# Kernel tuning notes

Measured on AMD Instinct MI355X. Metric: run time of the kernel, lower is better.

The kernel has to match this reference:

```python
import jax, jax.numpy as jnp
import numpy as np
import math

NUM_HEADS = 16

def get_slopes(n):
    def pow2(n):
        start = 2 ** (-2 ** (-(math.log2(n) - 3)))
        return [start * start ** i for i in range(n)]
    if math.log2(n).is_integer():
        return pow2(n)
    c = 2 ** math.floor(math.log2(n))
    return pow2(c) + get_slopes(2 * c)[0::2][: n - c]


def setup_inputs() -> dict:
    key = jax.random.key(0)
    ks = jax.random.split(key, 5)
    B, T, C = 2, 2048, 1024
    return {
        "x": jax.random.normal(ks[0], (B, T, C), dtype=jnp.float32),
        "W_qkv": jax.random.normal(ks[1], (C, 3 * C), dtype=jnp.float32) * 0.02,
        "b_qkv": jax.random.normal(ks[2], (3 * C,), dtype=jnp.float32) * 0.02,
        "W_proj": jax.random.normal(ks[3], (C, C), dtype=jnp.float32) * 0.02,
        "b_proj": jax.random.normal(ks[4], (C,), dtype=jnp.float32) * 0.02,
    }


def reference(x, W_qkv, b_qkv, W_proj, b_proj):
    B, T, C = x.shape
    H = NUM_HEADS
    D = C // H
    qkv = x @ W_qkv + b_qkv                       # [B,T,3C]
    q, k, v = jnp.split(qkv, 3, axis=-1)
    q = q.reshape(B, T, H, D).transpose(0, 2, 1, 3)  # [B,H,T,D]
    k = k.reshape(B, T, H, D).transpose(0, 2, 1, 3)
    v = v.reshape(B, T, H, D).transpose(0, 2, 1, 3)

    slopes = jnp.asarray(get_slopes(H), dtype=jnp.float32)  # [H]
    idx = jnp.arange(T)
    # alibi_bias(L).T in source: -(i-j) for j<=i, 0 for j>i  == min(j-i, 0)
    alibi = jnp.minimum(idx[None, :] - idx[:, None], 0).astype(jnp.float32)  # [T,T]
    bias = slopes[:, None, None] * alibi          # [H,T,T]

    scale = 1.0 / math.sqrt(D)
    scores = jnp.einsum("bhtd,bhsd->bhts", q, k) * scale + bias[None]
    # NOTE: source code builds a causal -inf mask but never adds it -> non-causal
    w = jax.nn.softmax(scores, axis=-1)
    y = jnp.einsum("bhts,bhsd->bhtd", w, v)       # [B,H,T,D]
    y = y.transpose(0, 2, 1, 3).reshape(B, T, C)
    return y @ W_proj + b_proj
```

## Files before the change

### kernel.cpp

```cpp
#include <hip/hip_runtime.h>
#include <hip/hip_bf16.h>
#include <cmath>
#include <cstdint>

typedef __bf16 bf16_t;
typedef __bf16 bf16x8 __attribute__((ext_vector_type(8)));
typedef float f32x4 __attribute__((ext_vector_type(4)));
typedef float f32x8 __attribute__((ext_vector_type(8)));

static_assert(sizeof(bf16x8) == 16, "bf16x8 must be 16B");

#define MFMA16(a, b, c) __builtin_amdgcn_mfma_f32_16x16x32_bf16((a), (b), (c), 0, 0, 0)

__device__ __forceinline__ void load_lds_16B(const bf16_t* gsrc, bf16_t* ldst) {
  __builtin_amdgcn_global_load_lds(
      (const __attribute__((address_space(1))) void*)gsrc,
      (__attribute__((address_space(3))) void*)ldst, 16, 0, 0);
}

__global__ void detect_dtype(const unsigned short* __restrict__ x,
                             int* __restrict__ flag) {
  const int lane = threadIdx.x;
  int cnt = 0;
#pragma unroll
  for (int t = 0; t < 8; ++t) {
    unsigned short u = x[2 * (lane + 64 * t)];
    int e = (u >> 7) & 0xFF;
    cnt += (e >= 90 && e <= 130) ? 1 : 0;
  }
#pragma unroll
  for (int off = 1; off < 64; off <<= 1) cnt += __shfl_xor(cnt, off, 64);
  if (lane == 0) *flag = (cnt < 300) ? 1 : 0;
}

__global__ __launch_bounds__(256) void convert_x(const void* __restrict__ x_,
                                                 bf16_t* __restrict__ xb,
                                                 const int* __restrict__ flagp) {
  const size_t idx = ((size_t)blockIdx.x * 256 + threadIdx.x) * 8;
  if (*flagp) {
    f32x8 v = *(const f32x8*)((const float*)x_ + idx);
    bf16x8 bv;
#pragma unroll
    for (int e = 0; e < 8; ++e) bv[e] = (bf16_t)v[e];
    *(bf16x8*)&xb[idx] = bv;
  } else {
    *(bf16x8*)&xb[idx] = *(const bf16x8*)((const bf16_t*)x_ + idx);
  }
}

__global__ __launch_bounds__(256) void wt_transpose(const void* __restrict__ W_,
                                                    bf16_t* __restrict__ Wt,
                                                    int K, int N,
                                                    const int* __restrict__ flagp) {
  __shared__ bf16_t tile[64 * 72];
  const int is_f32 = *flagp;
  const int tid = threadIdx.x;
  const int k0 = blockIdx.y * 64;
  const int n0 = blockIdx.x * 64;
  const int r = tid >> 3;
  const int c = (tid & 7) * 8;
#pragma unroll
  for (int t = 0; t < 2; ++t) {
    int rr = r + t * 32;
    if (is_f32) {
      const float* W = (const float*)W_;
      f32x8 v = *(const f32x8*)&W[(size_t)(k0 + rr) * N + n0 + c];
      bf16x8 bv;
#pragma unroll
      for (int e = 0; e < 8; ++e) bv[e] = (bf16_t)v[e];
      *(bf16x8*)&tile[rr * 72 + c] = bv;
    } else {
      const bf16_t* W = (const bf16_t*)W_;
      *(bf16x8*)&tile[rr * 72 + c] = *(const bf16x8*)&W[(size_t)(k0 + rr) * N + n0 + c];
    }
  }
  __syncthreads();
#pragma unroll
  for (int t = 0; t < 2; ++t) {
    int rr = r + t * 32;
    bf16x8 v;
#pragma unroll
    for (int e = 0; e < 8; ++e) v[e] = tile[(c + e) * 72 + rr];
    *(bf16x8*)&Wt[(size_t)(n0 + rr) * K + k0 + c] = v;
  }
}

__global__ __launch_bounds__(256, 2) void gemm_bt(
    const bf16_t* __restrict__ A, const bf16_t* __restrict__ Bt,
    const void* __restrict__ bias_, void* __restrict__ C_,
    bf16_t* __restrict__ qb, bf16_t* __restrict__ kb, bf16_t* __restrict__ vt,
    int M, int N, int K, int mode, const int* __restrict__ flagp) {
  __shared__ bf16_t As[128 * 64];
  __shared__ bf16_t Bs[128 * 64];
  const int is_f32 = *flagp;
  const int tid = threadIdx.x;
  const int wave = tid >> 6, lane = tid & 63;
  const int l16 = lane & 15, quad = lane >> 4;
  const int m0 = blockIdx.y * 128, n0 = blockIdx.x * 128;
  const int wm = (wave >> 1) * 64, wn = (wave & 1) * 64;
  const int lr = lane >> 3, lc = (lane & 7) * 8;
  f32x4 acc[4][4] = {};

  for (int k0 = 0; k0 < K; k0 += 64) {
#pragma unroll
    for (int t = 0; t < 4; ++t) {
      const int chunk = wave * 4 + t;
      const int row = chunk * 8 + lr;
      load_lds_16B(&A[(size_t)(m0 + row) * K + k0 + lc], &As[chunk * 512]);
      load_lds_16B(&Bt[(size_t)(n0 + row) * K + k0 + lc], &Bs[chunk * 512]);
    }
    __syncthreads();
#pragma unroll
    for (int ks = 0; ks < 2; ++ks) {
      bf16x8 af[4], bfr[4];
#pragma unroll
      for (int i = 0; i < 4; ++i) {
        af[i]  = *(const bf16x8*)&As[(wm + i * 16 + l16) * 64 + ks * 32 + quad * 8];
        bfr[i] = *(const bf16x8*)&Bs[(wn + i * 16 + l16) * 64 + ks * 32 + quad * 8];
      }
#pragma unroll
      for (int i = 0; i < 4; ++i)
#pragma unroll
        for (int j = 0; j < 4; ++j)
          acc[i][j] = MFMA16(af[i], bfr[j], acc[i][j]);
    }
    __syncthreads();
  }

#pragma unroll
  for (int j = 0; j < 4; ++j) {
    const int n = n0 + wn + j * 16 + l16;
    const float bv = is_f32 ? ((const float*)bias_)[n]
                            : (float)((const bf16_t*)bias_)[n];
    if (mode == 0) {
#pragma unroll
      for (int i = 0; i < 4; ++i)
#pragma unroll
        for (int r = 0; r < 4; ++r) {
          int m = m0 + wm + i * 16 + quad * 4 + r;
          float val = acc[i][j][r] + bv;
          if (is_f32) ((float*)C_)[(size_t)m * N + n] = val;
          else ((bf16_t*)C_)[(size_t)m * N + n] = (bf16_t)val;
        }
    } else {
      const int region = n >> 10;
      const int nn = n & 1023;
      const int hh = nn >> 6, dd = nn & 63;
#pragma unroll
      for (int i = 0; i < 4; ++i)
#pragma unroll
        for (int r = 0; r < 4; ++r) {
          int m = m0 + wm + i * 16 + quad * 4 + r;
          int bb = m >> 11, tt = m & 2047;
          size_t bh = (size_t)(bb * 16 + hh);
          float val = acc[i][j][r] + bv;
          if (region == 0)
            qb[(bh * 2048 + tt) * 64 + dd] = (bf16_t)val;
          else if (region == 1)
            kb[(bh * 2048 + tt) * 64 + dd] = (bf16_t)val;
          else
            vt[bh * 131072 + (size_t)dd * 2048 + tt] = (bf16_t)val;
        }
    }
  }
}

__global__ __launch_bounds__(512, 4) void attn_kernel(
    const bf16_t* __restrict__ qbuf, const bf16_t* __restrict__ kbuf,
    const bf16_t* __restrict__ vT, bf16_t* __restrict__ y) {
  const int T = 2048;
  __shared__ __align__(16) char smem[57344];
  bf16_t* Ks  = (bf16_t*)smem;
  bf16_t* VTs = (bf16_t*)(smem + 18432);
  bf16_t* Ps  = (bf16_t*)(smem + 36864);

  const int tid = threadIdx.x;
  const int wave = tid >> 6, lane = tid & 63;
  const int g2 = wave >> 2, wp = wave & 3;
  const int l16 = lane & 15, quad = lane >> 4;
  const int bh = blockIdx.y;
  const int b = bh >> 4, h = bh & 15;
  const int i0 = blockIdx.x * 128 + wp * 32;
  const float L2E = 1.44269504088896f;
  const float c1 = 0.125f * L2E;
  const float c2 = exp2f(-0.5f * (float)(h + 1)) * L2E;

  bf16x8 qf[2][2];
#pragma unroll
  for (int g = 0; g < 2; ++g) {
    const bf16_t* qrow = qbuf + ((size_t)bh * T + i0 + g * 16 + l16) * 64;
    qf[g][0] = *(const bf16x8*)&qrow[quad * 8];
    qf[g][1] = *(const bf16x8*)&qrow[32 + quad * 8];
  }

  f32x4 o[2][4] = {};
  float rsum[2][4] = {};

  const bf16_t* kbase = kbuf + (size_t)bh * T * 64;
  const bf16_t* vbase = vT + (size_t)bh * 64 * T;

  bf16_t* myKs = Ks + g2 * 4608;
  bf16_t* myVs = VTs + g2 * 4608;
  bf16_t* Pw = Ps + wave * 1280;

  const int gtid = tid & 255;
  const int sr = gtid >> 3, sc = (gtid & 7) * 8;
  const int jbase = g2 * 1024;

  for (int jj = 0; jj < 1024; jj += 64) {
    const int j0 = jbase + jj;
#pragma unroll
    for (int t = 0; t < 2; ++t) {
      int rr = sr + t * 32;
      *(bf16x8*)&myKs[rr * 72 + sc] = *(const bf16x8*)&kbase[(size_t)(j0 + rr) * 64 + sc];
      *(bf16x8*)&myVs[rr * 72 + sc] = *(const bf16x8*)&vbase[(size_t)rr * T + j0 + sc];
    }
    __syncthreads();

#pragma unroll
    for (int hl = 0; hl < 2; ++hl) {
      bf16x8 kf[2][2];
#pragma unroll
      for (int jtl = 0; jtl < 2; ++jtl) {
        const int jr = (hl * 2 + jtl) * 16 + l16;
        kf[jtl][0] = *(const bf16x8*)&myKs[jr * 72 + quad * 8];
        kf[jtl][1] = *(const bf16x8*)&myKs[jr * 72 + 32 + quad * 8];
      }
#pragma unroll
      for (int g = 0; g < 2; ++g) {
        f32x4 s[2] = {};
#pragma unroll
        for (int jtl = 0; jtl < 2; ++jtl) {
          s[jtl] = MFMA16(qf[g][0], kf[jtl][0], s[jtl]);
          s[jtl] = MFMA16(qf[g][1], kf[jtl][1], s[jtl]);
        }
        const float fb = (float)(i0 + g * 16 + quad * 4);
#pragma unroll
        for (int jtl = 0; jtl < 2; ++jtl) {
          const float jmf = (float)(j0 + (hl * 2 + jtl) * 16 + l16);
#pragma unroll
          for (int r = 0; r < 4; ++r) {
            float dm = fminf(jmf - (fb + (float)r), 0.0f);
            float p = exp2f(c1 * s[jtl][r] + c2 * dm);
            rsum[g][r] += p;
            Pw[(g * 16 + quad * 4 + r) * 40 + jtl * 16 + l16] = (bf16_t)p;
          }
        }
      }
      __asm__ volatile("s_waitcnt lgkmcnt(0)" ::: "memory");

      bf16x8 vf[4];
#pragma unroll
      for (int dt = 0; dt < 4; ++dt)
        vf[dt] = *(const bf16x8*)&myVs[(dt * 16 + l16) * 72 + hl * 32 + quad * 8];
#pragma unroll
      for (int g = 0; g < 2; ++g) {
        const bf16x8 pf = *(const bf16x8*)&Pw[(g * 16 + l16) * 40 + quad * 8];
#pragma unroll
        for (int dt = 0; dt < 4; ++dt)
          o[g][dt] = MFMA16(pf, vf[dt], o[g][dt]);
      }
    }
    __syncthreads();
  }

#pragma unroll
  for (int g = 0; g < 2; ++g)
#pragma unroll
    for (int r = 0; r < 4; ++r) {
      float s = rsum[g][r];
      s += __shfl_xor(s, 1, 64);
      s += __shfl_xor(s, 2, 64);
      s += __shfl_xor(s, 4, 64);
      s += __shfl_xor(s, 8, 64);
      rsum[g][r] = s;
    }

  __syncthreads();
  float* exO = (float*)smem;
  float* exR = (float*)(smem + 36864);
  if (g2 == 1) {
    float* myO = exO + wp * (32 * 65);
#pragma unroll
    for (int g = 0; g < 2; ++g)
#pragma unroll
      for (int dt = 0; dt < 4; ++dt)
#pragma unroll
        for (int r = 0; r < 4; ++r)
          myO[(g * 16 + quad * 4 + r) * 65 + dt * 16 + l16] = o[g][dt][r];
    if (l16 == 0) {
#pragma unroll
      for (int g = 0; g < 2; ++g)
#pragma unroll
        for (int r = 0; r < 4; ++r)
          exR[wp * 32 + g * 16 + quad * 4 + r] = rsum[g][r];
    }
  }
  __syncthreads();
  if (g2 == 0) {
    float* myO = exO + wp * (32 * 65);
#pragma unroll
    for (int g = 0; g < 2; ++g)
#pragma unroll
      for (int dt = 0; dt < 4; ++dt)
#pragma unroll
        for (int r = 0; r < 4; ++r) {
          const int row = g * 16 + quad * 4 + r;
          const float denom = rsum[g][r] + exR[wp * 32 + row];
          const float val = (o[g][dt][r] + myO[row * 65 + dt * 16 + l16]) / denom;
          const int ig = i0 + row;
          const int d = dt * 16 + l16;
          y[((size_t)(b * 2048 + ig)) * 1024 + h * 64 + d] = (bf16_t)val;
        }
  }
}

extern "C" void kernel_launch(void* const* d_in, const int* in_sizes, int n_in,
                              void* d_out, int out_size, void* d_ws, size_t ws_size,
                              hipStream_t stream) {
  const void* x     = d_in[0];
  const void* Wqkv  = d_in[1];
  const void* bqkv  = d_in[2];
  const void* Wproj = d_in[3];
  const void* bproj = d_in[4];

  const size_t SEG = (size_t)32 * 2048 * 64;
  bf16_t* ws = (bf16_t*)d_ws;
  bf16_t* qb = ws;
  bf16_t* kb = ws + SEG;
  bf16_t* vt = ws + 2 * SEG;
  bf16_t* yb = ws + 3 * SEG;
  bf16_t* WqkvT  = yb;
  bf16_t* WprojT = qb;
  bf16_t* xb = (bf16_t*)d_out;
  int* flag1 = (int*)((char*)d_ws + (size_t)31 * 1024 * 1024);
  int* flag2 = (int*)((char*)d_ws + (size_t)4 * 1024 * 1024);

  detect_dtype<<<1, 64, 0, stream>>>((const unsigned short*)x, flag1);
  wt_transpose<<<dim3(48, 16), 256, 0, stream>>>(Wqkv, WqkvT, 1024, 3072, flag1);
  convert_x<<<2048, 256, 0, stream>>>(x, xb, flag1);
  gemm_bt<<<dim3(24, 32), 256, 0, stream>>>(xb, WqkvT, bqkv, nullptr, qb, kb, vt,
                                            4096, 3072, 1024, 1, flag1);
  attn_kernel<<<dim3(16, 32), 512, 0, stream>>>(qb, kb, vt, yb);
  detect_dtype<<<1, 64, 0, stream>>>((const unsigned short*)x, flag2);
  wt_transpose<<<dim3(16, 16), 256, 0, stream>>>(Wproj, WprojT, 1024, 1024, flag2);
  gemm_bt<<<dim3(8, 32), 256, 0, stream>>>(yb, WprojT, bproj, d_out,
                                           nullptr, nullptr, nullptr,
                                           4096, 1024, 1024, 0, flag2);
}
```

Baseline: 250.9 us.

## Switch attention to 32x32 MFMA with register-resident P via permlane swap

Rewrites the attention inner loop to compute S transposed (K·Q) with 32x32x16 MFMAs, so the softmax probabilities stay in registers. They are converted to bf16 and rearranged across lanes with permlane32_swap to form the A operand for the PV MFMA, which removes the per-wave LDS staging buffer for P and its waitcnt. It also specialises the ALiBi bias per 32-key block into fully-unmasked, fully-biased and diagonal cases to cut fminf and bias arithmetic. Row sums now need only one cross-lane shuffle. The risk is correctness of the lane and row mapping, plus extra register pressure from the f32x16 accumulators.

Result: faster. 221.4 us (-11.8%).

```diff
diff --git a/kernel.cpp b/kernel.cpp
--- a/kernel.cpp
+++ b/kernel.cpp
@@ -7,10 +7,14 @@
 typedef __bf16 bf16x8 __attribute__((ext_vector_type(8)));
 typedef float f32x4 __attribute__((ext_vector_type(4)));
 typedef float f32x8 __attribute__((ext_vector_type(8)));
+typedef float f32x16 __attribute__((ext_vector_type(16)));
+typedef unsigned int u32x2 __attribute__((ext_vector_type(2)));
+typedef unsigned int u32x4 __attribute__((ext_vector_type(4)));
 
 static_assert(sizeof(bf16x8) == 16, "bf16x8 must be 16B");
 
 #define MFMA16(a, b, c) __builtin_amdgcn_mfma_f32_16x16x32_bf16((a), (b), (c), 0, 0, 0)
+#define MFMA32(a, b, c) __builtin_amdgcn_mfma_f32_32x32x16_bf16((a), (b), (c), 0, 0, 0)
 
 __device__ __forceinline__ void load_lds_16B(const bf16_t* gsrc, bf16_t* ldst) {
   __builtin_amdgcn_global_load_lds(
@@ -169,15 +173,14 @@
     const bf16_t* __restrict__ qbuf, const bf16_t* __restrict__ kbuf,
     const bf16_t* __restrict__ vT, bf16_t* __restrict__ y) {
   const int T = 2048;
-  __shared__ __align__(16) char smem[57344];
+  __shared__ __align__(16) char smem[36864];
   bf16_t* Ks  = (bf16_t*)smem;
   bf16_t* VTs = (bf16_t*)(smem + 18432);
-  bf16_t* Ps  = (bf16_t*)(smem + 36864);
 
   const int tid = threadIdx.x;
   const int wave = tid >> 6, lane = tid & 63;
   const int g2 = wave >> 2, wp = wave & 3;
-  const int l16 = lane & 15, quad = lane >> 4;
+  const int l32 = lane & 31, hi = lane >> 5;
   const int bh = blockIdx.y;
   const int b = bh >> 4, h = bh & 15;
   const int i0 = blockIdx.x * 128 + wp * 32;
@@ -185,27 +188,25 @@
   const float c1 = 0.125f * L2E;
   const float c2 = exp2f(-0.5f * (float)(h + 1)) * L2E;
 
-  bf16x8 qf[2][2];
-#pragma unroll
-  for (int g = 0; g < 2; ++g) {
-    const bf16_t* qrow = qbuf + ((size_t)bh * T + i0 + g * 16 + l16) * 64;
-    qf[g][0] = *(const bf16x8*)&qrow[quad * 8];
-    qf[g][1] = *(const bf16x8*)&qrow[32 + quad * 8];
-  }
-
-  f32x4 o[2][4] = {};
-  float rsum[2][4] = {};
+  bf16x8 qf[4];
+  {
+    const bf16_t* qrow = qbuf + ((size_t)bh * T + i0 + l32) * 64 + hi * 8;
+#pragma unroll
+    for (int kk = 0; kk < 4; ++kk) qf[kk] = *(const bf16x8*)&qrow[kk * 16];
+  }
+
+  f32x16 o[2] = {};
+  float rsum = 0.f;
 
   const bf16_t* kbase = kbuf + (size_t)bh * T * 64;
   const bf16_t* vbase = vT + (size_t)bh * 64 * T;
-
   bf16_t* myKs = Ks + g2 * 4608;
   bf16_t* myVs = VTs + g2 * 4608;
-  bf16_t* Pw = Ps + wave * 1280;
 
   const int gtid = tid & 255;
   const int sr = gtid >> 3, sc = (gtid & 7) * 8;
   const int jbase = g2 * 1024;
+  const float dif = (float)(4 * hi - i0 - l32);
 
   for (int jj = 0; jj < 1024; jj += 64) {
     const int j0 = jbase + jj;
@@ -219,99 +220,96 @@
 
 #pragma unroll
     for (int hl = 0; hl < 2; ++hl) {
-      bf16x8 kf[2][2];
-#pragma unroll
-      for (int jtl = 0; jtl < 2; ++jtl) {
-        const int jr = (hl * 2 + jtl) * 16 + l16;
-        kf[jtl][0] = *(const bf16x8*)&myKs[jr * 72 + quad * 8];
-        kf[jtl][1] = *(const bf16x8*)&myKs[jr * 72 + 32 + quad * 8];
-      }
-#pragma unroll
-      for (int g = 0; g < 2; ++g) {
-        f32x4 s[2] = {};
-#pragma unroll
-        for (int jtl = 0; jtl < 2; ++jtl) {
-          s[jtl] = MFMA16(qf[g][0], kf[jtl][0], s[jtl]);
-          s[jtl] = MFMA16(qf[g][1], kf[jtl][1], s[jtl]);
+      const int jblk = j0 + hl * 32;
+      f32x16 s = {};
+#pragma unroll
+      for (int kk = 0; kk < 4; ++kk) {
+        bf16x8 kf = *(const bf16x8*)&myKs[(hl * 32 + l32) * 72 + kk * 16 + hi * 8];
+        s = MFMA32(kf, qf[kk], s);
+      }
+
+      float rs = 0.f;
+      if (jblk >= i0 + 31) {
+#pragma unroll
+        for (int r = 0; r < 16; ++r) {
+          float p = exp2f(c1 * s[r]);
+          rs += p; s[r] = p;
         }
-        const float fb = (float)(i0 + g * 16 + quad * 4);
-#pragma unroll
-        for (int jtl = 0; jtl < 2; ++jtl) {
-          const float jmf = (float)(j0 + (hl * 2 + jtl) * 16 + l16);
-#pragma unroll
-          for (int r = 0; r < 4; ++r) {
-            float dm = fminf(jmf - (fb + (float)r), 0.0f);
-            float p = exp2f(c1 * s[jtl][r] + c2 * dm);
-            rsum[g][r] += p;
-            Pw[(g * 16 + quad * 4 + r) * 40 + jtl * 16 + l16] = (bf16_t)p;
+      } else {
+        const float cjb = c2 * ((float)jblk + dif);
+        if (jblk + 31 <= i0) {
+#pragma unroll
+          for (int r = 0; r < 16; ++r) {
+            const float kr = (float)((r & 3) + 8 * (r >> 2));
+            float p = exp2f(fmaf(c1, s[r], fmaf(c2, kr, cjb)));
+            rs += p; s[r] = p;
+          }
+        } else {
+#pragma unroll
+          for (int r = 0; r < 16; ++r) {
+            const float kr = (float)((r & 3) + 8 * (r >> 2));
+            float p = exp2f(fmaf(c1, s[r], fminf(fmaf(c2, kr, cjb), 0.f)));
+            rs += p; s[r] = p;
           }
         }
       }
-      __asm__ volatile("s_waitcnt lgkmcnt(0)" ::: "memory");
-
-      bf16x8 vf[4];
-#pragma unroll
-      for (int dt = 0; dt < 4; ++dt)
-        vf[dt] = *(const bf16x8*)&myVs[(dt * 16 + l16) * 72 + hl * 32 + quad * 8];
-#pragma unroll
-      for (int g = 0; g < 2; ++g) {
-        const bf16x8 pf = *(const bf16x8*)&Pw[(g * 16 + l16) * 40 + quad * 8];
-#pragma unroll
-        for (int dt = 0; dt < 4; ++dt)
-          o[g][dt] = MFMA16(pf, vf[dt], o[g][dt]);
+      rsum += rs;
+
+      unsigned int w[8];
+#pragma unroll
+      for (int q = 0; q < 8; ++q)
+        asm("v_cvt_pk_bf16_f32 %0, %1, %2"
+            : "=v"(w[q]) : "v"(s[2 * q]), "v"(s[2 * q + 1]));
+      u32x2 q02 = __builtin_amdgcn_permlane32_swap(w[0], w[2], false, false);
+      u32x2 q13 = __builtin_amdgcn_permlane32_swap(w[1], w[3], false, false);
+      u32x2 q46 = __builtin_amdgcn_permlane32_swap(w[4], w[6], false, false);
+      u32x2 q57 = __builtin_amdgcn_permlane32_swap(w[5], w[7], false, false);
+      u32x4 a0u = {q02[0], q13[0], q02[1], q13[1]};
+      u32x4 a1u = {q46[0], q57[0], q46[1], q57[1]};
+      bf16x8 af0 = __builtin_bit_cast(bf16x8, a0u);
+      bf16x8 af1 = __builtin_bit_cast(bf16x8, a1u);
+
+#pragma unroll
+      for (int db = 0; db < 2; ++db) {
+        bf16x8 v0 = *(const bf16x8*)&myVs[(db * 32 + l32) * 72 + hl * 32 + hi * 8];
+        o[db] = MFMA32(af0, v0, o[db]);
+        bf16x8 v1 = *(const bf16x8*)&myVs[(db * 32 + l32) * 72 + hl * 32 + 16 + hi * 8];
+        o[db] = MFMA32(af1, v1, o[db]);
       }
     }
     __syncthreads();
   }
 
-#pragma unroll
-  for (int g = 0; g < 2; ++g)
-#pragma unroll
-    for (int r = 0; r < 4; ++r) {
-      float s = rsum[g][r];
-      s += __shfl_xor(s, 1, 64);
-      s += __shfl_xor(s, 2, 64);
-      s += __shfl_xor(s, 4, 64);
-      s += __shfl_xor(s, 8, 64);
-      rsum[g][r] = s;
-    }
-
-  __syncthreads();
+  rsum += __shfl_xor(rsum, 32, 64);
+
   float* exO = (float*)smem;
-  float* exR = (float*)(smem + 36864);
+  float* exR = (float*)(smem + 33280);
   if (g2 == 1) {
     float* myO = exO + wp * (32 * 65);
 #pragma unroll
-    for (int g = 0; g < 2; ++g)
-#pragma unroll
-      for (int dt = 0; dt < 4; ++dt)
-#pragma unroll
-        for (int r = 0; r < 4; ++r)
-          myO[(g * 16 + quad * 4 + r) * 65 + dt * 16 + l16] = o[g][dt][r];
-    if (l16 == 0) {
-#pragma unroll
-      for (int g = 0; g < 2; ++g)
-#pragma unroll
-        for (int r = 0; r < 4; ++r)
-          exR[wp * 32 + g * 16 + quad * 4 + r] = rsum[g][r];
-    }
+    for (int db = 0; db < 2; ++db)
+#pragma unroll
+      for (int r = 0; r < 16; ++r) {
+        const int row = (r & 3) + 8 * (r >> 2) + 4 * hi;
+        myO[row * 65 + db * 32 + l32] = o[db][r];
+      }
+    if (lane < 32) exR[wp * 32 + lane] = rsum;
   }
   __syncthreads();
   if (g2 == 0) {
     float* myO = exO + wp * (32 * 65);
 #pragma unroll
-    for (int g = 0; g < 2; ++g)
-#pragma unroll
-      for (int dt = 0; dt < 4; ++dt)
-#pragma unroll
-        for (int r = 0; r < 4; ++r) {
-          const int row = g * 16 + quad * 4 + r;
-          const float denom = rsum[g][r] + exR[wp * 32 + row];
-          const float val = (o[g][dt][r] + myO[row * 65 + dt * 16 + l16]) / denom;
-          const int ig = i0 + row;
-          const int d = dt * 16 + l16;
-          y[((size_t)(b * 2048 + ig)) * 1024 + h * 64 + d] = (bf16_t)val;
-        }
+    for (int r = 0; r < 16; ++r) {
+      const int row = (r & 3) + 8 * (r >> 2) + 4 * hi;
+      const float denom = __shfl(rsum, row, 64) + exR[wp * 32 + row];
+      const float rden = 1.0f / denom;
+      const int ig = i0 + row;
+#pragma unroll
+      for (int db = 0; db < 2; ++db) {
+        const float val = (o[db][r] + myO[row * 65 + db * 32 + l32]) * rden;
+        y[((size_t)(b * 2048 + ig)) * 1024 + h * 64 + db * 32 + l32] = (bf16_t)val;
+      }
+    }
   }
 }
 
```
